# Optimization experiments

Hardware: AMD Instinct MI355X
Metric: run time of the kernel (lower is better)

## Reference

```python
import jax, jax.numpy as jnp
import numpy as np

EMBED = 768
HEADS = 12
HID = EMBED * HEADS  # 9216; head_dim == embed_dim in this module
EPS = 1e-5


def _layernorm(x, g, b):
    mu = jnp.mean(x, axis=-1, keepdims=True)
    var = jnp.mean(jnp.square(x - mu), axis=-1, keepdims=True)
    return (x - mu) * jax.lax.rsqrt(var + EPS) * g + b


def setup_inputs() -> dict:
    key = jax.random.key(0)
    ks = jax.random.split(key, 16)
    B, S = 4, 1024
    s_in = 1.0 / np.sqrt(EMBED)
    s_hid = 1.0 / np.sqrt(HID)
    return {
        "x": jax.random.normal(ks[0], (B, S, EMBED), jnp.float32),
        "ln1_g": jnp.ones((EMBED,), jnp.float32),
        "ln1_b": jnp.zeros((EMBED,), jnp.float32),
        "wq": jax.random.normal(ks[1], (EMBED, HID), jnp.float32) * s_in,
        "bq": jnp.zeros((HID,), jnp.float32),
        "wk": jax.random.normal(ks[2], (EMBED, HID), jnp.float32) * s_in,
        "bk": jnp.zeros((HID,), jnp.float32),
        "wv": jax.random.normal(ks[3], (EMBED, HID), jnp.float32) * s_in,
        "bv": jnp.zeros((HID,), jnp.float32),
        "wo": jax.random.normal(ks[4], (HID, EMBED), jnp.float32) * s_hid,
        "bo": jnp.zeros((EMBED,), jnp.float32),
        "ln2_g": jnp.ones((EMBED,), jnp.float32),
        "ln2_b": jnp.zeros((EMBED,), jnp.float32),
        "w1": jax.random.normal(ks[5], (EMBED, EMBED), jnp.float32) * s_in,
        "b1": jnp.zeros((EMBED,), jnp.float32),
        "w2": jax.random.normal(ks[6], (EMBED, EMBED), jnp.float32) * s_in,
        "b2": jnp.zeros((EMBED,), jnp.float32),
    }


def reference(x, ln1_g, ln1_b, wq, bq, wk, bk, wv, bv, wo, bo,
              ln2_g, ln2_b, w1, b1, w2, b2):
    B, S, D = x.shape
    H = HEADS
    nx = _layernorm(x, ln1_g, ln1_b)
    # QKV projections: each head gets a FULL embed_dim-wide slice (head_dim == D)
    q = (nx @ wq + bq).reshape(B, S, H, D)
    k = (nx @ wk + bk).reshape(B, S, H, D)
    v = (nx @ wv + bv).reshape(B, S, H, D)
    scores = jnp.einsum("bqhd,bkhd->bhqk", q, k) / jnp.sqrt(jnp.float32(D))
    # Original applies softmax over dim=1 of per-head [B,q,k] scores -> the QUERY axis
    attn = jax.nn.softmax(scores, axis=-2)
    ctx = jnp.einsum("bhqk,bkhd->bqhd", attn, v).reshape(B, S, H * D)
    x_att = ctx @ wo + bo
    x = x + x_att
    h = _layernorm(x, ln2_g, ln2_b)
    h = jax.nn.gelu(h @ w1 + b1, approximate=False)
    h = h @ w2 + b2
    return x + h
```

## Files before the change

kernel.cpp:

```cpp
#include <hip/hip_runtime.h>
#include <math.h>

#define D_EMB 768
#define HEADS 12
#define HID   9216
#define BATCH 4
#define SEQ   1024
#define M_ROWS 4096

typedef __attribute__((ext_vector_type(8))) short bf16x8;
typedef __attribute__((ext_vector_type(4))) float f32x4;

__device__ __forceinline__ float b2f(unsigned short u) {
    return __uint_as_float(((unsigned)u) << 16);
}
__device__ __forceinline__ unsigned short f2b(float f) {
    unsigned u = __float_as_uint(f);
    u += 0x7fffu + ((u >> 16) & 1u);
    return (unsigned short)(u >> 16);
}

__device__ __forceinline__ void async_copy16(const void* g, void* l) {
    __builtin_amdgcn_global_load_lds(
        (const __attribute__((address_space(1))) void*)g,
        (__attribute__((address_space(3))) void*)l, 16, 0, 0);
}

enum { EPI_BF16 = 0, EPI_SCALE_BF16 = 1, EPI_BIAS_BF16 = 2,
       EPI_BIAS_GELU_BF16 = 3, EPI_BIAS_RES_F32 = 4, EPI_F32_PART = 5 };

__global__ __launch_bounds__(512, 2)
void gemm_qkv8(const unsigned short* __restrict__ A,
               const unsigned short* __restrict__ B,
               unsigned short* __restrict__ Cq,
               unsigned short* __restrict__ Ck,
               unsigned short* __restrict__ Cv,
               const float* __restrict__ bq,
               const float* __restrict__ bk,
               const float* __restrict__ bv,
               int K, int lda, int ldb, int ldc)
{
    extern __shared__ unsigned short lds[];
    const int tid = threadIdx.x;
    const int lane = tid & 63;
    const int wid = tid >> 6;
    const int wm = wid >> 2;
    const int wn = wid & 3;
    const int bm = blockIdx.x, bn = blockIdx.y;

    const int r = lane & 15, ks = lane >> 4;
    const int swz_src = (((lane & 7) ^ (lane >> 3)) * 8);
    const int l8 = lane * 8;

    const unsigned short* Ag = A + (long)(bm * 256) * lda;
    const unsigned short* Bg = B + (long)(bn * 256) * ldb;

    auto ldsA = [&](int buf) -> unsigned short* { return lds + buf * 32768; };
    auto ldsB = [&](int buf) -> unsigned short* { return lds + buf * 32768 + 16384; };

    auto stageA = [&](int buf, int reg, int kt) {
        unsigned short* base = ldsA(buf);
        #pragma unroll
        for (int i = 0; i < 2; i++) {
            const int idx = i * 64 + wid * 8;
            const int row = (reg ? 64 : 0) + (idx & 63) + ((idx >> 6) << 7);
            const unsigned short* src = Ag + (long)(row + (lane >> 3)) * lda
                                        + kt * 64 + swz_src;
            async_copy16(src, base + row * 64 + l8);
        }
    };
    auto stageB = [&](int buf, int reg, int kt) {
        unsigned short* base = ldsB(buf);
        #pragma unroll
        for (int i = 0; i < 2; i++) {
            const int idx = i * 64 + wid * 8;
            const int row = ((idx >> 5) << 6) + (reg ? 32 : 0) + (idx & 31);
            const unsigned short* src = Bg + (long)(row + (lane >> 3)) * ldb
                                        + kt * 64 + swz_src;
            async_copy16(src, base + row * 64 + l8);
        }
    };
    auto readA = [&](int buf, int m, int s) {
        const int row = wm * 128 + m * 16 + r;
        const int cg = (ks + s * 4) ^ (lane & 7);
        return *(const bf16x8*)&ldsA(buf)[row * 64 + cg * 8];
    };
    auto readB = [&](int buf, int n, int s) {
        const int row = wn * 64 + n * 16 + r;
        const int cg = (ks + s * 4) ^ (lane & 7);
        return *(const bf16x8*)&ldsB(buf)[row * 64 + cg * 8];
    };

    f32x4 acc[8][4] = {};
    const int nt = K >> 6;

    stageA(0, 0, 0); stageB(0, 0, 0); stageB(0, 1, 0); stageA(0, 1, 0);
    if (nt > 1) { stageA(1, 0, 1); stageB(1, 0, 1); }
    asm volatile("s_waitcnt vmcnt(4)" ::: "memory");
    __builtin_amdgcn_s_barrier();

    for (int t = 0; t < nt; t++) {
        const int buf = t & 1, obuf = buf ^ 1;
        #pragma unroll
        for (int q = 0; q < 4; q++) {
            const int mq = q >> 1, nh = q & 1;
            if (q > 0 || t > 0) {
                asm volatile("s_waitcnt vmcnt(8)" ::: "memory");
                __builtin_amdgcn_s_barrier();
            }
            if (q == 0)      { if (t + 1 < nt) stageB(obuf, 1, t + 1); }
            else if (q == 1) { if (t + 1 < nt) stageA(obuf, 1, t + 1); }
            else if (q == 2) { if (t + 2 < nt) stageA(buf, 0, t + 2); }
            else             { if (t + 2 < nt) stageB(buf, 0, t + 2); }

            bf16x8 af[4][2], bfv[2][2];
            #pragma unroll
            for (int mi = 0; mi < 4; mi++)
                #pragma unroll
                for (int s = 0; s < 2; s++)
                    af[mi][s] = readA(buf, mq * 4 + mi, s);
            #pragma unroll
            for (int ni = 0; ni < 2; ni++)
                #pragma unroll
                for (int s = 0; s < 2; s++)
                    bfv[ni][s] = readB(buf, nh * 2 + ni, s);

            __builtin_amdgcn_s_setprio(1);
            #pragma unroll
            for (int mi = 0; mi < 4; mi++)
                #pragma unroll
                for (int ni = 0; ni < 2; ni++)
                    #pragma unroll
                    for (int s = 0; s < 2; s++)
                        acc[mq * 4 + mi][nh * 2 + ni] =
                            __builtin_amdgcn_mfma_f32_16x16x32_bf16(
                                af[mi][s], bfv[ni][s],
                                acc[mq * 4 + mi][nh * 2 + ni], 0, 0, 0);
            __builtin_amdgcn_s_setprio(0);
        }
    }

    const int third = (bn * 256) / ldc;
    unsigned short* C = (third == 0) ? Cq : (third == 1) ? Ck : Cv;
    const float* bs = (third == 0) ? bq : (third == 1) ? bk : bv;
    #pragma unroll
    for (int m = 0; m < 8; m++) {
        const int row0 = bm * 256 + wm * 128 + m * 16 + ks * 4;
        #pragma unroll
        for (int n = 0; n < 4; n++) {
            const int cl = bn * 256 + wn * 64 + n * 16 + r - third * ldc;
            const float bsv = bs[cl];
            #pragma unroll
            for (int j = 0; j < 4; j++)
                C[(long)(row0 + j) * ldc + cl] = f2b(acc[m][n][j] + bsv);
        }
    }
}

template<int EPI, int SWAP = 0, int XS = 0>
__global__ __launch_bounds__(256)
void gemm_bt(const unsigned short* __restrict__ A,
             const unsigned short* __restrict__ B,
             void* __restrict__ Cv,
             const float* __restrict__ bias,
             const float* __restrict__ resid,
             float scale, int K, int ksplit,
             int lda, int ldb, int ldc, int nh, int nbm, int nbn,
             long sAb, long sAh, long sBb, long sBh, long sCb, long sCh)
{
    __shared__ unsigned short As[2][128 * 32];
    __shared__ unsigned short Bs[2][128 * 32];

    int bm, bn, bz;
    if constexpr (XS) {
        const int lid = blockIdx.x;
        const int nb = nbm * nbn;
        const int xcd = lid & 7, j = lid >> 3;
        bz = xcd * ((4 * nh) >> 3) + j / nb;
        const int pos = j % nb;
        bm = pos / nbn;
        bn = pos % nbn;
    } else {
        bm = SWAP ? blockIdx.x : blockIdx.y;
        bn = SWAP ? blockIdx.y : blockIdx.x;
        bz = blockIdx.z;
    }

    int Kloop = K;
    const unsigned short* Ab;
    const unsigned short* Bb;
    long coff;
    if constexpr (EPI == EPI_F32_PART) {
        Ab = A + (long)bz * ksplit;
        Bb = B + (long)bz * ksplit;
        coff = (long)bz * sCb;
        Kloop = ksplit;
    } else {
        const int b = bz / nh, h = bz - b * nh;
        Ab = A + (long)b * sAb + (long)h * sAh;
        Bb = B + (long)b * sBb + (long)h * sBh;
        coff = (long)b * sCb + (long)h * sCh;
    }

    const int tid = threadIdx.x;
    const int c0 = tid, c1 = tid + 256;

    const unsigned short* Ap0 = Ab + (long)(bm * 128 + (c0 >> 2)) * lda + (c0 & 3) * 8;
    const unsigned short* Ap1 = Ab + (long)(bm * 128 + (c1 >> 2)) * lda + (c1 & 3) * 8;
    const unsigned short* Bp0 = Bb + (long)(bn * 128 + (c0 >> 2)) * ldb + (c0 & 3) * 8;
    const unsigned short* Bp1 = Bb + (long)(bn * 128 + (c1 >> 2)) * ldb + (c1 & 3) * 8;

    const int lane = tid & 63;
    const int wid = tid >> 6;
    const int wm = wid >> 1, wn = wid & 1;
    const int r = lane & 15, ks = lane >> 4;

    f32x4 acc[4][4] = {};

    async_copy16(Ap0, &As[0][c0 * 8]);
    async_copy16(Ap1, &As[0][c1 * 8]);
    async_copy16(Bp0, &Bs[0][c0 * 8]);
    async_copy16(Bp1, &Bs[0][c1 * 8]);
    Ap0 += 32; Ap1 += 32; Bp0 += 32; Bp1 += 32;
    __syncthreads();

    int cur = 0;
    for (int kt = 0; kt < Kloop; kt += 32) {
        if (kt + 32 < Kloop) {
            const int nxt = cur ^ 1;
            async_copy16(Ap0, &As[nxt][c0 * 8]);
            async_copy16(Ap1, &As[nxt][c1 * 8]);
            async_copy16(Bp0, &Bs[nxt][c0 * 8]);
            async_copy16(Bp1, &Bs[nxt][c1 * 8]);
            Ap0 += 32; Ap1 += 32; Bp0 += 32; Bp1 += 32;
        }

        bf16x8 af[4], bfr[4];
        #pragma unroll
        for (int m = 0; m < 4; m++)
            af[m] = *(const bf16x8*)&As[cur][(wm * 64 + m * 16 + r) * 32 + ks * 8];
        #pragma unroll
        for (int n = 0; n < 4; n++)
            bfr[n] = *(const bf16x8*)&Bs[cur][(wn * 64 + n * 16 + r) * 32 + ks * 8];

        #pragma unroll
        for (int m = 0; m < 4; m++)
            #pragma unroll
            for (int n = 0; n < 4; n++)
                acc[m][n] = __builtin_amdgcn_mfma_f32_16x16x32_bf16(
                    af[m], bfr[n], acc[m][n], 0, 0, 0);

        __syncthreads();
        cur ^= 1;
    }

    #pragma unroll
    for (int m = 0; m < 4; m++) {
        const int row0 = bm * 128 + wm * 64 + m * 16 + ks * 4;
        #pragma unroll
        for (int n = 0; n < 4; n++) {
            const int col = bn * 128 + wn * 64 + n * 16 + r;
            #pragma unroll
            for (int j = 0; j < 4; j++) {
                const int row = row0 + j;
                float v = acc[m][n][j];
                if constexpr (EPI == EPI_SCALE_BF16) v *= scale;
                if constexpr (EPI == EPI_BIAS_BF16 || EPI == EPI_BIAS_GELU_BF16 ||
                              EPI == EPI_BIAS_RES_F32) v += bias[col];
                if constexpr (EPI == EPI_BIAS_GELU_BF16)
                    v = 0.5f * v * (1.0f + erff(v * 0.70710678118654752f));
                if constexpr (EPI == EPI_BIAS_RES_F32) {
                    float* C = (float*)Cv;
                    C[coff + (long)row * ldc + col] = v + resid[(long)row * ldc + col];
                } else if constexpr (EPI == EPI_F32_PART) {
                    float* C = (float*)Cv;
                    C[coff + (long)row * ldc + col] = v;
                } else {
                    unsigned short* C = (unsigned short*)Cv;
                    C[coff + (long)row * ldc + col] = f2b(v);
                }
            }
        }
    }
}

__global__ __launch_bounds__(256)
void reduce_part(const f32x4* __restrict__ p, f32x4* __restrict__ x2,
                 int n4, int nsp)
{
    const int i = blockIdx.x * 256 + threadIdx.x;
    f32x4 a = x2[i];
    for (int s = 0; s < nsp; s++) {
        const f32x4 v = p[(long)s * n4 + i];
        a[0] += v[0]; a[1] += v[1]; a[2] += v[2]; a[3] += v[3];
    }
    x2[i] = a;
}

__global__ __launch_bounds__(256)
void transpose_w(const float* __restrict__ in, unsigned short* __restrict__ out,
                 int R, int C, int col0)
{
    __shared__ float t[32][33];
    const int c0 = blockIdx.x * 32, r0 = blockIdx.y * 32;
    const int tx = threadIdx.x & 31, ty = threadIdx.x >> 5;
    #pragma unroll
    for (int i = 0; i < 4; i++)
        t[ty + i * 8][tx] = in[(long)(r0 + ty + i * 8) * C + col0 + c0 + tx];
    __syncthreads();
    #pragma unroll
    for (int i = 0; i < 4; i++)
        out[(long)(c0 + ty + i * 8) * R + r0 + tx] = f2b(t[tx][ty + i * 8]);
}

__global__ __launch_bounds__(256)
void transpose_v(const unsigned short* __restrict__ v, unsigned short* __restrict__ vt,
                 int ng)
{
    __shared__ unsigned short t[32][34];
    const int bz = blockIdx.z;
    const int b = bz / ng, hl = bz - b * ng;
    const int d0 = blockIdx.x * 32, s0 = blockIdx.y * 32;
    const int tx = threadIdx.x & 31, ty = threadIdx.x >> 5;
    const int ld = ng * D_EMB;
    const unsigned short* vin = v + (long)b * SEQ * ld + (long)hl * D_EMB;
    #pragma unroll
    for (int i = 0; i < 4; i++)
        t[ty + i * 8][tx] = vin[(long)(s0 + ty + i * 8) * ld + d0 + tx];
    __syncthreads();
    unsigned short* vo = vt + (long)bz * D_EMB * SEQ;
    #pragma unroll
    for (int i = 0; i < 4; i++)
        vo[(long)(d0 + ty + i * 8) * SEQ + s0 + tx] = t[tx][ty + i * 8];
}

__global__ __launch_bounds__(256)
void ln_kernel(const float* __restrict__ x, const float* __restrict__ g,
               const float* __restrict__ bb, unsigned short* __restrict__ out)
{
    const int row = blockIdx.x;
    const float* xr = x + (long)row * D_EMB;
    const int t = threadIdx.x;
    float v0 = xr[t], v1 = xr[t + 256], v2 = xr[t + 512];
    float s = v0 + v1 + v2;
    float ss = v0 * v0 + v1 * v1 + v2 * v2;
    #pragma unroll
    for (int o = 32; o > 0; o >>= 1) {
        s += __shfl_down(s, o);
        ss += __shfl_down(ss, o);
    }
    __shared__ float red[8];
    __shared__ float mu_s, rs_s;
    const int wid = t >> 6;
    if ((t & 63) == 0) { red[wid] = s; red[4 + wid] = ss; }
    __syncthreads();
    if (t == 0) {
        float a = red[0] + red[1] + red[2] + red[3];
        float q = red[4] + red[5] + red[6] + red[7];
        float mu = a * (1.0f / D_EMB);
        float var = q * (1.0f / D_EMB) - mu * mu;
        mu_s = mu;
        rs_s = rsqrtf(var + 1e-5f);
    }
    __syncthreads();
    const float mu = mu_s, rs = rs_s;
    unsigned short* orow = out + (long)row * D_EMB;
    orow[t]       = f2b((v0 - mu) * rs * g[t]       + bb[t]);
    orow[t + 256] = f2b((v1 - mu) * rs * g[t + 256] + bb[t + 256]);
    orow[t + 512] = f2b((v2 - mu) * rs * g[t + 512] + bb[t + 512]);
}

__global__ __launch_bounds__(256)
void x2_init(const float* __restrict__ x, const float* __restrict__ bo,
             float* __restrict__ x2)
{
    const int row = blockIdx.x;
    const float* xr = x + (long)row * D_EMB;
    float* o = x2 + (long)row * D_EMB;
    const int t = threadIdx.x;
    o[t]       = xr[t]       + bo[t];
    o[t + 256] = xr[t + 256] + bo[t + 256];
    o[t + 512] = xr[t + 512] + bo[t + 512];
}

__global__ __launch_bounds__(256)
void col_softmax(unsigned short* __restrict__ s)
{
    const long base = (long)blockIdx.y * ((long)SEQ * SEQ);
    const int t63 = threadIdx.x & 63;
    const int part = threadIdx.x >> 6;
    const int col = blockIdx.x * 64 + t63;
    unsigned short* p = s + base + col;
    const int q0 = part * 256;
    float m = -1e30f, sum = 0.0f;
    for (int q = q0; q < q0 + 256; q++) {
        float v = b2f(p[(long)q * SEQ]);
        float mn = fmaxf(m, v);
        sum = sum * __expf(m - mn) + __expf(v - mn);
        m = mn;
    }
    __shared__ float lm[4][64], ls[4][64];
    lm[part][t63] = m;
    ls[part][t63] = sum;
    __syncthreads();
    const float M = fmaxf(fmaxf(lm[0][t63], lm[1][t63]),
                          fmaxf(lm[2][t63], lm[3][t63]));
    const float S = ls[0][t63] * __expf(lm[0][t63] - M)
                  + ls[1][t63] * __expf(lm[1][t63] - M)
                  + ls[2][t63] * __expf(lm[2][t63] - M)
                  + ls[3][t63] * __expf(lm[3][t63] - M);
    const float inv = 1.0f / S;
    for (int q = q0; q < q0 + 256; q++) {
        float v = b2f(p[(long)q * SEQ]);
        p[(long)q * SEQ] = f2b(__expf(v - M) * inv);
    }
}

extern "C" void kernel_launch(void* const* d_in, const int* in_sizes, int n_in,
                              void* d_out, int out_size, void* d_ws, size_t ws_size,
                              hipStream_t stream)
{
    const float* x    = (const float*)d_in[0];
    const float* ln1g = (const float*)d_in[1];
    const float* ln1b = (const float*)d_in[2];
    const float* wq   = (const float*)d_in[3];
    const float* bq   = (const float*)d_in[4];
    const float* wk   = (const float*)d_in[5];
    const float* bk   = (const float*)d_in[6];
    const float* wv   = (const float*)d_in[7];
    const float* bv   = (const float*)d_in[8];
    const float* wo   = (const float*)d_in[9];
    const float* bo   = (const float*)d_in[10];
    const float* ln2g = (const float*)d_in[11];
    const float* ln2b = (const float*)d_in[12];
    const float* w1   = (const float*)d_in[13];
    const float* b1   = (const float*)d_in[14];
    const float* w2   = (const float*)d_in[15];
    const float* b2   = (const float*)d_in[16];
    float* out = (float*)d_out;

    auto a256 = [](size_t b) { return (b + 255) & ~(size_t)255; };

    auto plan_bytes = [&](int g) -> size_t {
        size_t o = 0;
        o += a256((size_t)D_EMB * D_EMB * 2);
        o += a256((size_t)D_EMB * D_EMB * 2);
        o += a256((size_t)M_ROWS * D_EMB * 2);
        o += a256((size_t)M_ROWS * D_EMB * 2);
        o += a256((size_t)M_ROWS * D_EMB * 4);
        o += a256((size_t)3 * g * D_EMB * D_EMB * 2);
        o += 3 * a256((size_t)M_ROWS * (size_t)g * D_EMB * 2);
        size_t vr = (size_t)M_ROWS * (size_t)g * D_EMB * 2;
        size_t sc = (size_t)BATCH * g * SEQ * SEQ * 2;
        o += a256(vr > sc ? vr : sc);
        return o;
    };
    const int cand[6] = {12, 6, 4, 3, 2, 1};
    int G = 1;
    for (int i = 0; i < 6; i++) {
        if (plan_bytes(cand[i]) <= ws_size) { G = cand[i]; break; }
    }
    const int NG = G * D_EMB;

    char* ws = (char*)d_ws;
    size_t off = 0;
    auto alloc = [&](size_t bytes) {
        void* p = ws + off;
        off += a256(bytes);
        return p;
    };
    unsigned short* w1T = (unsigned short*)alloc((size_t)D_EMB * D_EMB * 2);
    unsigned short* w2T = (unsigned short*)alloc((size_t)D_EMB * D_EMB * 2);
    unsigned short* nx  = (unsigned short*)alloc((size_t)M_ROWS * D_EMB * 2);
    unsigned short* h1  = (unsigned short*)alloc((size_t)M_ROWS * D_EMB * 2);
    float* x2           = (float*)alloc((size_t)M_ROWS * D_EMB * 4);
    unsigned short* wsl = (unsigned short*)alloc((size_t)3 * NG * D_EMB * 2);
    unsigned short* qg  = (unsigned short*)alloc((size_t)M_ROWS * NG * 2);
    unsigned short* kg  = (unsigned short*)alloc((size_t)M_ROWS * NG * 2);
    unsigned short* vtg = (unsigned short*)alloc((size_t)M_ROWS * NG * 2);
    {
        size_t vr = (size_t)M_ROWS * NG * 2;
        size_t sc = (size_t)BATCH * G * SEQ * SEQ * 2;
        (void)alloc(vr > sc ? vr : sc);
    }
    unsigned short* vr  = vtg + (size_t)M_ROWS * NG;
    unsigned short* scg = vr;
    unsigned short* ctx = qg;

    const size_t part_one = (size_t)M_ROWS * D_EMB * 4;
    const size_t avail = 2 * (size_t)M_ROWS * NG * 2;
    int nsp = 4;
    while (nsp > 1 && (size_t)nsp * part_one > avail) nsp >>= 1;
    while (nsp > 1 && (NG / nsp) % 32 != 0) nsp >>= 1;
    float* part = (float*)kg;

    const dim3 blk(256);
    const float scl = 0.03608439182435161f;
    const int nbh = BATCH * G;
    const bool xs_ok = (nbh % 8) == 0;

    static bool attr_set = false;
    if (!attr_set) {
        hipFuncSetAttribute((const void*)gemm_qkv8,
                            hipFuncAttributeMaxDynamicSharedMemorySize, 131072);
        attr_set = true;
    }

    ln_kernel<<<dim3(M_ROWS), blk, 0, stream>>>(x, ln1g, ln1b, nx);
    x2_init<<<dim3(M_ROWS), blk, 0, stream>>>(x, bo, x2);
    transpose_w<<<dim3(D_EMB / 32, D_EMB / 32), blk, 0, stream>>>(w1, w1T, D_EMB, D_EMB, 0);
    transpose_w<<<dim3(D_EMB / 32, D_EMB / 32), blk, 0, stream>>>(w2, w2T, D_EMB, D_EMB, 0);

    const int ngrp = HEADS / G;
    for (int g = 0; g < ngrp; g++) {
        const int h0 = g * G;
        unsigned short* wslQ = wsl;
        unsigned short* wslK = wsl + (size_t)NG * D_EMB;
        unsigned short* wslV = wsl + (size_t)2 * NG * D_EMB;
        transpose_w<<<dim3(NG / 32, D_EMB / 32), blk, 0, stream>>>(wq, wslQ, D_EMB, HID, h0 * D_EMB);
        transpose_w<<<dim3(NG / 32, D_EMB / 32), blk, 0, stream>>>(wk, wslK, D_EMB, HID, h0 * D_EMB);
        transpose_w<<<dim3(NG / 32, D_EMB / 32), blk, 0, stream>>>(wv, wslV, D_EMB, HID, h0 * D_EMB);

        gemm_qkv8<<<dim3(M_ROWS / 256, 3 * NG / 256, 1), dim3(512), 131072, stream>>>(
            nx, wsl, qg, kg, vr,
            bq + h0 * D_EMB, bk + h0 * D_EMB, bv + h0 * D_EMB,
            D_EMB, D_EMB, D_EMB, NG);
        transpose_v<<<dim3(D_EMB / 32, SEQ / 32, nbh), blk, 0, stream>>>(vr, vtg, G);

        if (xs_ok) {
            gemm_bt<EPI_SCALE_BF16, 0, 1><<<dim3(nbh * 64, 1, 1), blk, 0, stream>>>(
                qg, kg, scg, nullptr, nullptr,
                scl, D_EMB, 0, NG, NG, SEQ, G, 8, 8,
                (long)SEQ * NG, D_EMB, (long)SEQ * NG, D_EMB,
                (long)G * SEQ * SEQ, (long)SEQ * SEQ);
        } else {
            gemm_bt<EPI_SCALE_BF16><<<dim3(SEQ / 128, SEQ / 128, nbh), blk, 0, stream>>>(
                qg, kg, scg, nullptr, nullptr,
                scl, D_EMB, 0, NG, NG, SEQ, G, 0, 0,
                (long)SEQ * NG, D_EMB, (long)SEQ * NG, D_EMB,
                (long)G * SEQ * SEQ, (long)SEQ * SEQ);
        }

        col_softmax<<<dim3(SEQ / 64, nbh), blk, 0, stream>>>(scg);

        if (xs_ok) {
            gemm_bt<EPI_BF16, 0, 1><<<dim3(nbh * 48, 1, 1), blk, 0, stream>>>(
                scg, vtg, ctx, nullptr, nullptr,
                1.0f, SEQ, 0, SEQ, SEQ, NG, G, 8, 6,
                (long)G * SEQ * SEQ, (long)SEQ * SEQ,
                (long)G * D_EMB * SEQ, (long)D_EMB * SEQ,
                (long)SEQ * NG, (long)D_EMB);
        } else {
            gemm_bt<EPI_BF16><<<dim3(D_EMB / 128, SEQ / 128, nbh), blk, 0, stream>>>(
                scg, vtg, ctx, nullptr, nullptr,
                1.0f, SEQ, 0, SEQ, SEQ, NG, G, 0, 0,
                (long)G * SEQ * SEQ, (long)SEQ * SEQ,
                (long)G * D_EMB * SEQ, (long)D_EMB * SEQ,
                (long)SEQ * NG, (long)D_EMB);
        }

        transpose_w<<<dim3(D_EMB / 32, NG / 32), blk, 0, stream>>>(
            wo + (long)h0 * D_EMB * D_EMB, wsl, NG, D_EMB, 0);
        gemm_bt<EPI_F32_PART><<<dim3(D_EMB / 128, M_ROWS / 128, nsp), blk, 0, stream>>>(
            ctx, wsl, part, nullptr, nullptr,
            1.0f, NG, NG / nsp, NG, NG, D_EMB, 1, 0, 0,
            0, 0, 0, 0, (long)M_ROWS * D_EMB, 0);
        reduce_part<<<dim3(M_ROWS * D_EMB / 4 / 256), blk, 0, stream>>>(
            (const f32x4*)part, (f32x4*)x2, M_ROWS * D_EMB / 4, nsp);
    }

    ln_kernel<<<dim3(M_ROWS), blk, 0, stream>>>(x2, ln2g, ln2b, nx);

    gemm_bt<EPI_BIAS_GELU_BF16><<<dim3(D_EMB / 128, M_ROWS / 128, 1), blk, 0, stream>>>(
        nx, w1T, h1, b1, nullptr,
        1.0f, D_EMB, 0, D_EMB, D_EMB, D_EMB, 1, 0, 0, 0, 0, 0, 0, 0, 0);

    gemm_bt<EPI_BIAS_RES_F32><<<dim3(D_EMB / 128, M_ROWS / 128, 1), blk, 0, stream>>>(
        h1, w2T, out, b2, x2,
        1.0f, D_EMB, 0, D_EMB, D_EMB, D_EMB, 1, 0, 0, 0, 0, 0, 0, 0, 0);
}
```

Before: 801.1 us.

## Generalize 256x256 8-wave GEMM and use it for attention score and context GEMMs

The 512-thread, 256x256-tile QKV GEMM kernel gains batched/head strides, an XCD-aware block remap, and scale/plain bf16 epilogues. It then replaces the 128x128-tile gemm_bt for the QK^T score GEMM and the attn·V context GEMM. Larger tiles give more data reuse per LDS load and use the async global-to-LDS pipeline. The cost is fewer blocks per launch (nbh*16 and nbh*12), which may underfill the GPU. hipFuncSetAttribute is now called on every invocation instead of once.

After: 826.3 us. 1.03x slower.

```diff
diff --git a/kernel.cpp b/kernel.cpp
--- a/kernel.cpp
+++ b/kernel.cpp
@@ -28,17 +28,21 @@
 
 enum { EPI_BF16 = 0, EPI_SCALE_BF16 = 1, EPI_BIAS_BF16 = 2,
        EPI_BIAS_GELU_BF16 = 3, EPI_BIAS_RES_F32 = 4, EPI_F32_PART = 5 };
-
+enum { G8_QKV = 0, G8_SCALE = 1, G8_BF16 = 2 };
+
+template<int EPI, int XS>
 __global__ __launch_bounds__(512, 2)
-void gemm_qkv8(const unsigned short* __restrict__ A,
-               const unsigned short* __restrict__ B,
-               unsigned short* __restrict__ Cq,
-               unsigned short* __restrict__ Ck,
-               unsigned short* __restrict__ Cv,
-               const float* __restrict__ bq,
-               const float* __restrict__ bk,
-               const float* __restrict__ bv,
-               int K, int lda, int ldb, int ldc)
+void gemm8(const unsigned short* __restrict__ A,
+           const unsigned short* __restrict__ B,
+           void* __restrict__ C0,
+           void* __restrict__ C1,
+           void* __restrict__ C2,
+           const float* __restrict__ bq,
+           const float* __restrict__ bk,
+           const float* __restrict__ bv,
+           float scale, int K, int lda, int ldb, int ldc,
+           int nh, int nbm, int nbn,
+           long sAb, long sAh, long sBb, long sBh, long sCb, long sCh)
 {
     extern __shared__ unsigned short lds[];
     const int tid = threadIdx.x;
@@ -46,14 +50,28 @@
     const int wid = tid >> 6;
     const int wm = wid >> 2;
     const int wn = wid & 3;
-    const int bm = blockIdx.x, bn = blockIdx.y;
+
+    int bm, bn, bz;
+    if constexpr (XS) {
+        const int lid = blockIdx.x;
+        const int nb = nbm * nbn;
+        const int xcd = lid & 7, j = lid >> 3;
+        bz = xcd * ((4 * nh) >> 3) + j / nb;
+        const int pos = j % nb;
+        bm = pos / nbn;
+        bn = pos % nbn;
+    } else {
+        bm = blockIdx.x; bn = blockIdx.y; bz = blockIdx.z;
+    }
+    const int b = bz / nh, h = bz - b * nh;
 
     const int r = lane & 15, ks = lane >> 4;
     const int swz_src = (((lane & 7) ^ (lane >> 3)) * 8);
     const int l8 = lane * 8;
 
-    const unsigned short* Ag = A + (long)(bm * 256) * lda;
-    const unsigned short* Bg = B + (long)(bn * 256) * ldb;
+    const unsigned short* Ag = A + (long)b * sAb + (long)h * sAh + (long)(bm * 256) * lda;
+    const unsigned short* Bg = B + (long)b * sBb + (long)h * sBh + (long)(bn * 256) * ldb;
+    const long coff = (long)b * sCb + (long)h * sCh;
 
     auto ldsA = [&](int buf) -> unsigned short* { return lds + buf * 32768; };
     auto ldsB = [&](int buf) -> unsigned short* { return lds + buf * 32768 + 16384; };
@@ -103,7 +121,7 @@
         const int buf = t & 1, obuf = buf ^ 1;
         #pragma unroll
         for (int q = 0; q < 4; q++) {
-            const int mq = q >> 1, nh = q & 1;
+            const int mq = q >> 1, nq = q & 1;
             if (q > 0 || t > 0) {
                 asm volatile("s_waitcnt vmcnt(8)" ::: "memory");
                 __builtin_amdgcn_s_barrier();
@@ -123,7 +141,7 @@
             for (int ni = 0; ni < 2; ni++)
                 #pragma unroll
                 for (int s = 0; s < 2; s++)
-                    bfv[ni][s] = readB(buf, nh * 2 + ni, s);
+                    bfv[ni][s] = readB(buf, nq * 2 + ni, s);
 
             __builtin_amdgcn_s_setprio(1);
             #pragma unroll
@@ -132,32 +150,52 @@
                 for (int ni = 0; ni < 2; ni++)
                     #pragma unroll
                     for (int s = 0; s < 2; s++)
-                        acc[mq * 4 + mi][nh * 2 + ni] =
+                        acc[mq * 4 + mi][nq * 2 + ni] =
                             __builtin_amdgcn_mfma_f32_16x16x32_bf16(
                                 af[mi][s], bfv[ni][s],
-                                acc[mq * 4 + mi][nh * 2 + ni], 0, 0, 0);
+                                acc[mq * 4 + mi][nq * 2 + ni], 0, 0, 0);
             __builtin_amdgcn_s_setprio(0);
         }
     }
 
-    const int third = (bn * 256) / ldc;
-    unsigned short* C = (third == 0) ? Cq : (third == 1) ? Ck : Cv;
-    const float* bs = (third == 0) ? bq : (third == 1) ? bk : bv;
-    #pragma unroll
-    for (int m = 0; m < 8; m++) {
-        const int row0 = bm * 256 + wm * 128 + m * 16 + ks * 4;
-        #pragma unroll
-        for (int n = 0; n < 4; n++) {
-            const int cl = bn * 256 + wn * 64 + n * 16 + r - third * ldc;
-            const float bsv = bs[cl];
+    if constexpr (EPI == G8_QKV) {
+        const int third = (bn * 256) / ldc;
+        unsigned short* C = (third == 0) ? (unsigned short*)C0
+                          : (third == 1) ? (unsigned short*)C1
+                                         : (unsigned short*)C2;
+        const float* bs = (third == 0) ? bq : (third == 1) ? bk : bv;
+        #pragma unroll
+        for (int m = 0; m < 8; m++) {
+            const int row0 = bm * 256 + wm * 128 + m * 16 + ks * 4;
             #pragma unroll
-            for (int j = 0; j < 4; j++)
-                C[(long)(row0 + j) * ldc + cl] = f2b(acc[m][n][j] + bsv);
-        }
-    }
-}
-
-template<int EPI, int SWAP = 0, int XS = 0>
+            for (int n = 0; n < 4; n++) {
+                const int cl = bn * 256 + wn * 64 + n * 16 + r - third * ldc;
+                const float bsv = bs[cl];
+                #pragma unroll
+                for (int j = 0; j < 4; j++)
+                    C[(long)(row0 + j) * ldc + cl] = f2b(acc[m][n][j] + bsv);
+            }
+        }
+    } else {
+        unsigned short* C = (unsigned short*)C0;
+        #pragma unroll
+        for (int m = 0; m < 8; m++) {
+            const int row0 = bm * 256 + wm * 128 + m * 16 + ks * 4;
+            #pragma unroll
+            for (int n = 0; n < 4; n++) {
+                const int col = bn * 256 + wn * 64 + n * 16 + r;
+                #pragma unroll
+                for (int j = 0; j < 4; j++) {
+                    float v = acc[m][n][j];
+                    if constexpr (EPI == G8_SCALE) v *= scale;
+                    C[coff + (long)(row0 + j) * ldc + col] = f2b(v);
+                }
+            }
+        }
+    }
+}
+
+template<int EPI, int SWAP = 0>
 __global__ __launch_bounds__(256)
 void gemm_bt(const unsigned short* __restrict__ A,
              const unsigned short* __restrict__ B,
@@ -165,26 +203,15 @@
              const float* __restrict__ bias,
              const float* __restrict__ resid,
              float scale, int K, int ksplit,
-             int lda, int ldb, int ldc, int nh, int nbm, int nbn,
+             int lda, int ldb, int ldc, int nh,
              long sAb, long sAh, long sBb, long sBh, long sCb, long sCh)
 {
     __shared__ unsigned short As[2][128 * 32];
     __shared__ unsigned short Bs[2][128 * 32];
 
-    int bm, bn, bz;
-    if constexpr (XS) {
-        const int lid = blockIdx.x;
-        const int nb = nbm * nbn;
-        const int xcd = lid & 7, j = lid >> 3;
-        bz = xcd * ((4 * nh) >> 3) + j / nb;
-        const int pos = j % nb;
-        bm = pos / nbn;
-        bn = pos % nbn;
-    } else {
-        bm = SWAP ? blockIdx.x : blockIdx.y;
-        bn = SWAP ? blockIdx.y : blockIdx.x;
-        bz = blockIdx.z;
-    }
+    const int bm = SWAP ? blockIdx.x : blockIdx.y;
+    const int bn = SWAP ? blockIdx.y : blockIdx.x;
+    const int bz = blockIdx.z;
 
     int Kloop = K;
     const unsigned short* Ab;
@@ -499,12 +526,16 @@
     const int nbh = BATCH * G;
     const bool xs_ok = (nbh % 8) == 0;
 
-    static bool attr_set = false;
-    if (!attr_set) {
-        hipFuncSetAttribute((const void*)gemm_qkv8,
-                            hipFuncAttributeMaxDynamicSharedMemorySize, 131072);
-        attr_set = true;
-    }
+    hipFuncSetAttribute((const void*)gemm8<G8_QKV, 0>,
+                        hipFuncAttributeMaxDynamicSharedMemorySize, 131072);
+    hipFuncSetAttribute((const void*)gemm8<G8_SCALE, 1>,
+                        hipFuncAttributeMaxDynamicSharedMemorySize, 131072);
+    hipFuncSetAttribute((const void*)gemm8<G8_BF16, 1>,
+                        hipFuncAttributeMaxDynamicSharedMemorySize, 131072);
+    hipFuncSetAttribute((const void*)gemm8<G8_SCALE, 0>,
+                        hipFuncAttributeMaxDynamicSharedMemorySize, 131072);
+    hipFuncSetAttribute((const void*)gemm8<G8_BF16, 0>,
+                        hipFuncAttributeMaxDynamicSharedMemorySize, 131072);
 
     ln_kernel<<<dim3(M_ROWS), blk, 0, stream>>>(x, ln1g, ln1b, nx);
     x2_init<<<dim3(M_ROWS), blk, 0, stream>>>(x, bo, x2);
@@ -521,22 +552,23 @@
         transpose_w<<<dim3(NG / 32, D_EMB / 32), blk, 0, stream>>>(wk, wslK, D_EMB, HID, h0 * D_EMB);
         transpose_w<<<dim3(NG / 32, D_EMB / 32), blk, 0, stream>>>(wv, wslV, D_EMB, HID, h0 * D_EMB);
 
-        gemm_qkv8<<<dim3(M_ROWS / 256, 3 * NG / 256, 1), dim3(512), 131072, stream>>>(
+        gemm8<G8_QKV, 0><<<dim3(M_ROWS / 256, 3 * NG / 256, 1), dim3(512), 131072, stream>>>(
             nx, wsl, qg, kg, vr,
             bq + h0 * D_EMB, bk + h0 * D_EMB, bv + h0 * D_EMB,
-            D_EMB, D_EMB, D_EMB, NG);
+            1.0f, D_EMB, D_EMB, D_EMB, NG, 1, 0, 0,
+            0, 0, 0, 0, 0, 0);
         transpose_v<<<dim3(D_EMB / 32, SEQ / 32, nbh), blk, 0, stream>>>(vr, vtg, G);
 
         if (xs_ok) {
-            gemm_bt<EPI_SCALE_BF16, 0, 1><<<dim3(nbh * 64, 1, 1), blk, 0, stream>>>(
-                qg, kg, scg, nullptr, nullptr,
-                scl, D_EMB, 0, NG, NG, SEQ, G, 8, 8,
+            gemm8<G8_SCALE, 1><<<dim3(nbh * 16, 1, 1), dim3(512), 131072, stream>>>(
+                qg, kg, scg, nullptr, nullptr, nullptr, nullptr, nullptr,
+                scl, D_EMB, NG, NG, SEQ, G, 4, 4,
                 (long)SEQ * NG, D_EMB, (long)SEQ * NG, D_EMB,
                 (long)G * SEQ * SEQ, (long)SEQ * SEQ);
         } else {
-            gemm_bt<EPI_SCALE_BF16><<<dim3(SEQ / 128, SEQ / 128, nbh), blk, 0, stream>>>(
-                qg, kg, scg, nullptr, nullptr,
-                scl, D_EMB, 0, NG, NG, SEQ, G, 0, 0,
+            gemm8<G8_SCALE, 0><<<dim3(4, 4, nbh), dim3(512), 131072, stream>>>(
+                qg, kg, scg, nullptr, nullptr, nullptr, nullptr, nullptr,
+                scl, D_EMB, NG, NG, SEQ, G, 4, 4,
                 (long)SEQ * NG, D_EMB, (long)SEQ * NG, D_EMB,
                 (long)G * SEQ * SEQ, (long)SEQ * SEQ);
         }
@@ -544,16 +576,16 @@
         col_softmax<<<dim3(SEQ / 64, nbh), blk, 0, stream>>>(scg);
 
         if (xs_ok) {
-            gemm_bt<EPI_BF16, 0, 1><<<dim3(nbh * 48, 1, 1), blk, 0, stream>>>(
-                scg, vtg, ctx, nullptr, nullptr,
-                1.0f, SEQ, 0, SEQ, SEQ, NG, G, 8, 6,
+            gemm8<G8_BF16, 1><<<dim3(nbh * 12, 1, 1), dim3(512), 131072, stream>>>(
+                scg, vtg, ctx, nullptr, nullptr, nullptr, nullptr, nullptr,
+                1.0f, SEQ, SEQ, SEQ, NG, G, 4, 3,
                 (long)G * SEQ * SEQ, (long)SEQ * SEQ,
                 (long)G * D_EMB * SEQ, (long)D_EMB * SEQ,
                 (long)SEQ * NG, (long)D_EMB);
         } else {
-            gemm_bt<EPI_BF16><<<dim3(D_EMB / 128, SEQ / 128, nbh), blk, 0, stream>>>(
-                scg, vtg, ctx, nullptr, nullptr,
-                1.0f, SEQ, 0, SEQ, SEQ, NG, G, 0, 0,
+            gemm8<G8_BF16, 0><<<dim3(4, 3, nbh), dim3(512), 131072, stream>>>(
+                scg, vtg, ctx, nullptr, nullptr, nullptr, nullptr, nullptr,
+                1.0f, SEQ, SEQ, SEQ, NG, G, 4, 3,
                 (long)G * SEQ * SEQ, (long)SEQ * SEQ,
                 (long)G * D_EMB * SEQ, (long)D_EMB * SEQ,
                 (long)SEQ * NG, (long)D_EMB);
@@ -563,7 +595,7 @@
             wo + (long)h0 * D_EMB * D_EMB, wsl, NG, D_EMB, 0);
         gemm_bt<EPI_F32_PART><<<dim3(D_EMB / 128, M_ROWS / 128, nsp), blk, 0, stream>>>(
             ctx, wsl, part, nullptr, nullptr,
-            1.0f, NG, NG / nsp, NG, NG, D_EMB, 1, 0, 0,
+            1.0f, NG, NG / nsp, NG, NG, D_EMB, 1,
             0, 0, 0, 0, (long)M_ROWS * D_EMB, 0);
         reduce_part<<<dim3(M_ROWS * D_EMB / 4 / 256), blk, 0, stream>>>(
             (const f32x4*)part, (f32x4*)x2, M_ROWS * D_EMB / 4, nsp);
@@ -573,9 +605,9 @@
 
     gemm_bt<EPI_BIAS_GELU_BF16><<<dim3(D_EMB / 128, M_ROWS / 128, 1), blk, 0, stream>>>(
         nx, w1T, h1, b1, nullptr,
-        1.0f, D_EMB, 0, D_EMB, D_EMB, D_EMB, 1, 0, 0, 0, 0, 0, 0, 0, 0);
+        1.0f, D_EMB, 0, D_EMB, D_EMB, D_EMB, 1, 0, 0, 0, 0, 0, 0);
 
     gemm_bt<EPI_BIAS_RES_F32><<<dim3(D_EMB / 128, M_ROWS / 128, 1), blk, 0, stream>>>(
         h1, w2T, out, b2, x2,
-        1.0f, D_EMB, 0, D_EMB, D_EMB, D_EMB, 1, 0, 0, 0, 0, 0, 0, 0, 0);
-}
+        1.0f, D_EMB, 0, D_EMB, D_EMB, D_EMB, 1, 0, 0, 0, 0, 0, 0);
+}
```
